# Kernel optimization log

Hardware: AMD Instinct MI355X
Metric: run time of the kernel (lower is better)

The kernel has to match this reference:

```python
import jax, jax.numpy as jnp
import numpy as np

B, N, K = 1024, 200, 32
HID = 36
IN_DIM = K * (K + 2)  # k + q + flattened outer product


def setup_inputs() -> dict:
    key = jax.random.key(0)
    ks = jax.random.split(key, 4)
    candidate_ad = jax.random.normal(ks[0], (B, K), dtype=jnp.float32)
    goods = jax.random.normal(ks[1], (B, N, K), dtype=jnp.float32)
    W1 = jax.random.normal(ks[2], (IN_DIM, HID), dtype=jnp.float32) * (1.0 / np.sqrt(IN_DIM))
    b1 = jnp.zeros((HID,), dtype=jnp.float32)
    W2 = jax.random.normal(ks[3], (HID, 1), dtype=jnp.float32) * (1.0 / np.sqrt(HID))
    b2 = jnp.zeros((1,), dtype=jnp.float32)
    return {"candidate_ad": candidate_ad, "goods": goods, "W1": W1, "b1": b1, "W2": W2, "b2": b2}


def reference(candidate_ad, goods, W1, b1, W2, b2):
    # candidate_ad: [B, K] (attention key k), goods: [B, N, K] (queries q per item)
    Bs, Ns, Ks = goods.shape
    # outer product per item: einsum('bi,bj->bij', k, q) vectorized over N -> [B, N, K, K]
    outer = jnp.einsum('bi,bnj->bnij', candidate_ad, goods).reshape(Bs, Ns, Ks * Ks)
    k_b = jnp.broadcast_to(candidate_ad[:, None, :], (Bs, Ns, Ks))
    h1 = jnp.concatenate((k_b, goods, outer), axis=-1)          # [B, N, K*(K+2)]
    act = jax.nn.sigmoid(h1 @ W1 + b1)                           # [B, N, HID]
    weight = act @ W2 + b2                                       # [B, N, 1]
    out = jnp.sum(goods * weight, axis=1)                        # [B, K]
    return out
```

## Files before the change

kernel.cpp:

```cpp
#include <hip/hip_runtime.h>


#define BB 1024
#define BPB 4
#define NN 200
#define KK 32
#define HID 36
#define QP 40
#define LOG2E 1.44269504f

typedef __attribute__((ext_vector_type(8))) short bf16x8;
typedef __attribute__((ext_vector_type(4))) float f32x4;

__device__ __forceinline__ float rfl(float x) {
    return __uint_as_float(__builtin_amdgcn_readfirstlane(__float_as_uint(x)));
}
__device__ __forceinline__ unsigned short f2bf(float x) {
    unsigned int u = __float_as_uint(x);
    u = (u + 0x7fffu + ((u >> 16) & 1u)) >> 16;
    return (unsigned short)u;
}
__device__ __forceinline__ unsigned int pk_bf16(float lo, float hi) {
    unsigned int r;
    asm("v_cvt_pk_bf16_f32 %0, %1, %2" : "=v"(r) : "v"(lo), "v"(hi));
    return r;
}
__device__ __forceinline__ float fast_rcp(float x) {
#if __has_builtin(__builtin_amdgcn_rcpf)
    return __builtin_amdgcn_rcpf(x);
#else
    return 1.0f / x;
#endif
}
__device__ __forceinline__ float fast_exp2(float x) {
#if __has_builtin(__builtin_amdgcn_exp2f)
    return __builtin_amdgcn_exp2f(x);
#else
    return exp2f(x);
#endif
}

__global__ __launch_bounds__(1024, 4) void din_kernel(
    const float* __restrict__ cad,
    const float* __restrict__ goods,
    const float* __restrict__ W1,
    const float* __restrict__ b1p,
    const float* __restrict__ W2,
    const float* __restrict__ b2p,
    float* __restrict__ out)
{
    __shared__ alignas(16) unsigned short V16[BPB][48 * QP];
    __shared__ alignas(16) float c48[BPB * 48];
    __shared__ alignas(16) float w248[48];
    __shared__ alignas(16) float red_s[16 * KK];

    const int tid  = threadIdx.x;
    const int b0   = blockIdx.x * BPB;
    const int lane = tid & 63;
    const int wv   = tid >> 6;
    const int l15  = lane & 15, lk = lane >> 4;
    const int bsel = wv & 3;
    const int mrow = wv >> 2;

    const float* gbw = goods + (size_t)(b0 + bsel) * NN * KK;
    const float* k0p = cad + b0 * KK;
    const float* k1p = k0p + KK;
    const float* k2p = k1p + KK;
    const float* k3p = k2p + KK;

    const float b2v = rfl(b2p[0]);

    const float4* W1q = reinterpret_cast<const float4*>(W1);
    if (tid < 288) {
        float4 acc0 = W1q[288 + tid];
        float4 acc1 = acc0, acc2 = acc0, acc3 = acc0;
        #pragma unroll 4
        for (int i = 0; i < KK; ++i) {
            const float4 w0 = W1q[576 + 288 * i + tid];
            const float ki0 = k0p[i], ki1 = k1p[i], ki2 = k2p[i], ki3 = k3p[i];
            acc0.x += ki0 * w0.x; acc0.y += ki0 * w0.y;
            acc0.z += ki0 * w0.z; acc0.w += ki0 * w0.w;
            acc1.x += ki1 * w0.x; acc1.y += ki1 * w0.y;
            acc1.z += ki1 * w0.z; acc1.w += ki1 * w0.w;
            acc2.x += ki2 * w0.x; acc2.y += ki2 * w0.y;
            acc2.z += ki2 * w0.z; acc2.w += ki2 * w0.w;
            acc3.x += ki3 * w0.x; acc3.y += ki3 * w0.y;
            acc3.z += ki3 * w0.z; acc3.w += ki3 * w0.w;
        }
        const float a0[4] = {acc0.x, acc0.y, acc0.z, acc0.w};
        const float a1[4] = {acc1.x, acc1.y, acc1.z, acc1.w};
        const float a2[4] = {acc2.x, acc2.y, acc2.z, acc2.w};
        const float a3[4] = {acc3.x, acc3.y, acc3.z, acc3.w};
        #pragma unroll
        for (int q = 0; q < 4; ++q) {
            const int e = 4 * tid + q, j = e / 36, h = e - 36 * j;
            const int o = h * QP + j;
            V16[0][o] = f2bf(a0[q]);
            V16[1][o] = f2bf(a1[q]);
            V16[2][o] = f2bf(a2[q]);
            V16[3][o] = f2bf(a3[q]);
        }
    } else if (tid < 324) {
        const int u = tid - 288, bl = u / 9, hq = u % 9;
        const float* kp = cad + (b0 + bl) * KK;
        float4 acc = reinterpret_cast<const float4*>(b1p)[hq];
        #pragma unroll 4
        for (int i = 0; i < KK; ++i) {
            const float ki = kp[i];
            const float4 wc = W1q[i * 9 + hq];
            acc.x += ki * wc.x; acc.y += ki * wc.y;
            acc.z += ki * wc.z; acc.w += ki * wc.w;
        }
        float4 cp4;
        cp4.x = -acc.x * LOG2E; cp4.y = -acc.y * LOG2E;
        cp4.z = -acc.z * LOG2E; cp4.w = -acc.w * LOG2E;
        *reinterpret_cast<float4*>(&c48[bl * 48 + 4 * hq]) = cp4;
    } else if (tid < 336) {
        const int u = tid - 324, bl = u / 3, q = u % 3;
        *reinterpret_cast<float4*>(&c48[bl * 48 + 36 + 4 * q]) =
            make_float4(0.f, 0.f, 0.f, 0.f);
    } else if (tid < 348) {
        const int u = tid - 336;
        if (u < 9)
            *reinterpret_cast<float4*>(&w248[4 * u]) =
                reinterpret_cast<const float4*>(W2)[u];
        else
            *reinterpret_cast<float4*>(&w248[36 + 4 * (u - 9)]) =
                make_float4(0.f, 0.f, 0.f, 0.f);
    } else if (tid < 732) {
        const int p = tid - 348;
        const int word = p % 192, pair = p / 192;
        const int w = (36 + (word >> 4)) * (QP / 2) + (word & 15);
        reinterpret_cast<unsigned int*>(V16[2 * pair + 0])[w] = 0u;
        reinterpret_cast<unsigned int*>(V16[2 * pair + 1])[w] = 0u;
    }
    __syncthreads();

    bf16x8 bfr[3];
    #pragma unroll
    for (int nt = 0; nt < 3; ++nt)
        bfr[nt] = *reinterpret_cast<const bf16x8*>(&V16[bsel][(nt * 16 + l15) * QP + lk * 8]);
    const float* cb = c48 + bsel * 48;

    float facc[8] = {0.f, 0.f, 0.f, 0.f, 0.f, 0.f, 0.f, 0.f};

    auto tile = [&](const float4& qa, const float4& qb, int m, bool masked) {
        union { unsigned int u[4]; bf16x8 v; } aq;
        aq.u[0] = pk_bf16(qa.x, qa.y);
        aq.u[1] = pk_bf16(qa.z, qa.w);
        aq.u[2] = pk_bf16(qb.x, qb.y);
        aq.u[3] = pk_bf16(qb.z, qb.w);
        const f32x4 zero = {0.f, 0.f, 0.f, 0.f};
        const f32x4 d0 = __builtin_amdgcn_mfma_f32_16x16x32_bf16(bfr[0], aq.v, zero, 0, 0, 0);
        const f32x4 d1 = __builtin_amdgcn_mfma_f32_16x16x32_bf16(bfr[1], aq.v, zero, 0, 0, 0);
        const f32x4 d2 = __builtin_amdgcn_mfma_f32_16x16x32_bf16(bfr[2], aq.v, zero, 0, 0, 0);

        const f32x4 c0 = *reinterpret_cast<const f32x4*>(cb + lk * 4);
        const f32x4 w0 = *reinterpret_cast<const f32x4*>(&w248[lk * 4]);
        const f32x4 c1 = *reinterpret_cast<const f32x4*>(cb + 16 + lk * 4);
        const f32x4 w1 = *reinterpret_cast<const f32x4*>(&w248[16 + lk * 4]);
        const f32x4 c2 = *reinterpret_cast<const f32x4*>(cb + 32 + lk * 4);
        const f32x4 w2 = *reinterpret_cast<const f32x4*>(&w248[32 + lk * 4]);

        float p = 0.f;
        #pragma unroll
        for (int r = 0; r < 4; ++r) {
            p += fast_rcp(1.0f + fast_exp2(__builtin_fmaf(d0[r], -LOG2E, c0[r]))) * w0[r];
            p += fast_rcp(1.0f + fast_exp2(__builtin_fmaf(d1[r], -LOG2E, c1[r]))) * w1[r];
            p += fast_rcp(1.0f + fast_exp2(__builtin_fmaf(d2[r], -LOG2E, c2[r]))) * w2[r];
        }
        p += __shfl_xor(p, 16, 64);
        p += __shfl_xor(p, 32, 64);

        float wn = b2v + p;
        if (masked) {
            const int n = m * 16 + l15;
            wn = (n < NN) ? wn : 0.f;
        }
        facc[0] += qa.x * wn; facc[1] += qa.y * wn;
        facc[2] += qa.z * wn; facc[3] += qa.w * wn;
        facc[4] += qb.x * wn; facc[5] += qb.y * wn;
        facc[6] += qb.z * wn; facc[7] += qb.w * wn;
    };

    #pragma unroll
    for (int t = 0; t < 4; ++t) {
        const int m = mrow + 4 * t;
        if (m < 13) {
            int row = m * 16 + l15;
            row = (row < NN) ? row : (NN - 1);
            const float4* qp = reinterpret_cast<const float4*>(gbw + row * KK + lk * 8);
            tile(qp[0], qp[1], m, m == 12);
        }
    }

    #pragma unroll
    for (int s = 1; s <= 8; s <<= 1) {
        #pragma unroll
        for (int u = 0; u < 8; ++u)
            facc[u] += __shfl_xor(facc[u], s, 64);
    }
    if (l15 == 0) {
        #pragma unroll
        for (int u = 0; u < 8; ++u)
            red_s[(bsel * 4 + mrow) * KK + lk * 8 + u] = facc[u];
    }
    __syncthreads();

    if (tid < BPB * KK) {
        const int bl = tid >> 5, j = tid & 31;
        float s = 0.f;
        #pragma unroll
        for (int g = 0; g < 4; ++g) s += red_s[(bl * 4 + g) * KK + j];
        out[(b0 + bl) * KK + j] = s;
    }
}

extern "C" void kernel_launch(void* const* d_in, const int* in_sizes, int n_in,
                              void* d_out, int out_size, void* d_ws, size_t ws_size,
                              hipStream_t stream) {
    const float* cad   = (const float*)d_in[0];
    const float* goods = (const float*)d_in[1];
    const float* W1    = (const float*)d_in[2];
    const float* b1    = (const float*)d_in[3];
    const float* W2    = (const float*)d_in[4];
    const float* b2    = (const float*)d_in[5];
    float* outp = (float*)d_out;

    din_kernel<<<BB / BPB, 1024, 0, stream>>>(cad, goods, W1, b1, W2, b2, outp);
}
```

Measured before the change: 15.41 us.

## Prefetch goods tiles into LDS asynchronously during weight prologue

Waves 6-15 issue global_load_lds DMA copies of the block's whole goods slice (about 100KB) into dynamic shared memory with an XOR swizzle, before the W1/bias prologue runs. The main loop then reads q rows from LDS through the matching swizzle instead of from global memory. The aim is to hide the goods load latency behind the prologue compute. In exchange, LDS use per block grows a lot, which means a dynamic shared memory attribute must be set, and correctness relies on the DMA completing before the barrier.

Measured after the change: 15.30 us. About the same (-0.7%).

```diff
diff --git a/kernel.cpp b/kernel.cpp
--- a/kernel.cpp
+++ b/kernel.cpp
@@ -8,6 +8,13 @@
 #define HID 36
 #define QP 40
 #define LOG2E 1.44269504f
+
+#define QBYTES (BPB * NN * KK * 4)
+#define VOFF   QBYTES
+#define COFF   (VOFF + 15360)
+#define WOFF   (COFF + 768)
+#define ROFF   (WOFF + 192)
+#define SMEM_TOTAL (ROFF + 2048)
 
 typedef __attribute__((ext_vector_type(8))) short bf16x8;
 typedef __attribute__((ext_vector_type(4))) float f32x4;
@@ -49,10 +56,12 @@
     const float* __restrict__ b2p,
     float* __restrict__ out)
 {
-    __shared__ alignas(16) unsigned short V16[BPB][48 * QP];
-    __shared__ alignas(16) float c48[BPB * 48];
-    __shared__ alignas(16) float w248[48];
-    __shared__ alignas(16) float red_s[16 * KK];
+    extern __shared__ char smem[];
+    char*           Qlds = smem;
+    unsigned short* V16  = (unsigned short*)(smem + VOFF);
+    float*          c48  = (float*)(smem + COFF);
+    float*          w248 = (float*)(smem + WOFF);
+    float*          red_s = (float*)(smem + ROFF);
 
     const int tid  = threadIdx.x;
     const int b0   = blockIdx.x * BPB;
@@ -62,12 +71,24 @@
     const int bsel = wv & 3;
     const int mrow = wv >> 2;
 
-    const float* gbw = goods + (size_t)(b0 + bsel) * NN * KK;
+    if (wv >= 6) {
+        const char* gsrc = (const char*)(goods + (size_t)b0 * NN * KK);
+        const int loff = (lane * 16) ^ ((lane >> 3) << 4);
+        const int ubase = (wv - 6) * 10;
+        #pragma unroll
+        for (int j = 0; j < 10; ++j) {
+            const int u = ubase + j;
+            __builtin_amdgcn_global_load_lds(
+                (const __attribute__((address_space(1))) void*)(gsrc + u * 1024 + loff),
+                (__attribute__((address_space(3))) void*)(Qlds + u * 1024),
+                16, 0, 0);
+        }
+    }
+
     const float* k0p = cad + b0 * KK;
     const float* k1p = k0p + KK;
     const float* k2p = k1p + KK;
     const float* k3p = k2p + KK;
-
     const float b2v = rfl(b2p[0]);
 
     const float4* W1q = reinterpret_cast<const float4*>(W1);
@@ -95,10 +116,10 @@
         for (int q = 0; q < 4; ++q) {
             const int e = 4 * tid + q, j = e / 36, h = e - 36 * j;
             const int o = h * QP + j;
-            V16[0][o] = f2bf(a0[q]);
-            V16[1][o] = f2bf(a1[q]);
-            V16[2][o] = f2bf(a2[q]);
-            V16[3][o] = f2bf(a3[q]);
+            V16[0 * 1920 + o] = f2bf(a0[q]);
+            V16[1 * 1920 + o] = f2bf(a1[q]);
+            V16[2 * 1920 + o] = f2bf(a2[q]);
+            V16[3 * 1920 + o] = f2bf(a3[q]);
         }
     } else if (tid < 324) {
         const int u = tid - 288, bl = u / 9, hq = u % 9;
@@ -131,15 +152,16 @@
         const int p = tid - 348;
         const int word = p % 192, pair = p / 192;
         const int w = (36 + (word >> 4)) * (QP / 2) + (word & 15);
-        reinterpret_cast<unsigned int*>(V16[2 * pair + 0])[w] = 0u;
-        reinterpret_cast<unsigned int*>(V16[2 * pair + 1])[w] = 0u;
+        ((unsigned int*)V16)[(2 * pair + 0) * 960 + w] = 0u;
+        ((unsigned int*)V16)[(2 * pair + 1) * 960 + w] = 0u;
     }
     __syncthreads();
 
     bf16x8 bfr[3];
     #pragma unroll
     for (int nt = 0; nt < 3; ++nt)
-        bfr[nt] = *reinterpret_cast<const bf16x8*>(&V16[bsel][(nt * 16 + l15) * QP + lk * 8]);
+        bfr[nt] = *reinterpret_cast<const bf16x8*>(
+            V16 + bsel * 1920 + (nt * 16 + l15) * QP + lk * 8);
     const float* cb = c48 + bsel * 48;
 
     float facc[8] = {0.f, 0.f, 0.f, 0.f, 0.f, 0.f, 0.f, 0.f};
@@ -189,8 +211,12 @@
         if (m < 13) {
             int row = m * 16 + l15;
             row = (row < NN) ? row : (NN - 1);
-            const float4* qp = reinterpret_cast<const float4*>(gbw + row * KK + lk * 8);
-            tile(qp[0], qp[1], m, m == 12);
+            const int rlin  = bsel * NN + row;
+            const int byte0 = rlin * 128 + lk * 32;
+            const int swz   = (rlin & 7) << 4;
+            const float4 qa = *reinterpret_cast<const float4*>(Qlds + (byte0 ^ swz));
+            const float4 qb = *reinterpret_cast<const float4*>(Qlds + ((byte0 + 16) ^ swz));
+            tile(qa, qb, m, m == 12);
         }
     }
 
@@ -227,5 +253,13 @@
     const float* b2    = (const float*)d_in[5];
     float* outp = (float*)d_out;
 
-    din_kernel<<<BB / BPB, 1024, 0, stream>>>(cad, goods, W1, b1, W2, b2, outp);
-}
+    static bool attr_set = false;
+    if (!attr_set) {
+        (void)hipFuncSetAttribute((const void*)din_kernel,
+                                  hipFuncAttributeMaxDynamicSharedMemorySize,
+                                  SMEM_TOTAL);
+        attr_set = true;
+    }
+
+    din_kernel<<<BB / BPB, 1024, SMEM_TOTAL, stream>>>(cad, goods, W1, b1, W2, b2, outp);
+}
```
